# Optimization experiments

Measured on AMD Instinct MI355X. Metric: run time of the kernel, lower is better.

Reference implementation:

```python
import jax, jax.numpy as jnp
import numpy as np

B, N, D = 32, 4096, 256
K, Dc = 128, 64  # Dc = D_sq // K (per-cluster residual dim)
NEG_SLOPE = 0.01  # LeakyReLU default
EPS = 1e-12       # F.normalize default eps


def setup_inputs() -> dict:
    key = jax.random.key(0)
    ks = jax.random.split(key, 7)
    s = 0.05
    return {
        "descriptors": jax.random.normal(ks[0], (B, N, D), dtype=jnp.float32),
        # squeeze: Linear(D, Dc) -> LeakyReLU -> Linear(Dc, Dc)
        "W1": jax.random.normal(ks[1], (Dc, D), dtype=jnp.float32) * s,
        "b1": jnp.zeros((Dc,), dtype=jnp.float32),
        "W2": jax.random.normal(ks[2], (Dc, Dc), dtype=jnp.float32) * s,
        "b2": jnp.zeros((Dc,), dtype=jnp.float32),
        # assign: Linear(D, K) -> Softmax
        "Wa": jax.random.normal(ks[3], (K, D), dtype=jnp.float32) * s,
        "ba": jnp.zeros((K,), dtype=jnp.float32),
        # centroids (K, Dc)
        "centroid": jax.random.normal(ks[4], (K, Dc), dtype=jnp.float32),
    }


def reference(descriptors, W1, b1, W2, b2, Wa, ba, centroid):
    # squeeze MLP: (B,N,D) -> (B,N,Dc)
    h = jnp.einsum('bnd,ed->bne', descriptors, W1) + b1
    h = jnp.where(h >= 0, h, NEG_SLOPE * h)
    sq = jnp.einsum('bne,fe->bnf', h, W2) + b2
    # soft assignment: (B,N,K)
    assign = jax.nn.softmax(jnp.einsum('bnd,kd->bnk', descriptors, Wa) + ba, axis=-1)
    # VLAD: sum_n assign[b,n,k] * (sq[b,n,:] - centroid[k,:])
    # decomposed algebraically to avoid the (B,N,K,Dc) intermediate
    agg = jnp.einsum('bnd,bnk->bkd', sq, assign)          # (B,K,Dc)
    mass = assign.sum(axis=1)                              # (B,K)
    vlad = agg - mass[:, :, None] * centroid               # (B,K,Dc)
    out = vlad.reshape(B, K * Dc)
    norm = jnp.linalg.norm(out, axis=1, keepdims=True)
    return out / jnp.maximum(norm, EPS)
```

## Files before the change

kernel.cpp:

```cpp
#include <hip/hip_runtime.h>


#define B_   32
#define N_   4096
#define D_   256
#define K_   128
#define DC_  64
#define ITERS 16
#define NEG  0.01f

typedef __attribute__((ext_vector_type(8))) short bf16x8;
typedef __attribute__((ext_vector_type(4))) float f32x4;

#define XF_OFF   0
#define AT_OFF   16384
#define HB_OFF   24576
#define W2F_OFF  28672
#define MS_OFF   36864
#define LDS_BYTES 37888

__device__ __forceinline__ unsigned short f2bf(float x) {
  union { float f; unsigned u; } v; v.f = x;
  unsigned r = v.u + 0x7fffu + ((v.u >> 16) & 1u);
  return (unsigned short)(r >> 16);
}
__device__ __forceinline__ unsigned pack2(float a, float b) {
  return (unsigned)f2bf(a) | ((unsigned)f2bf(b) << 16);
}
__device__ __forceinline__ bf16x8 ldf(const char* s, int off) {
  return *reinterpret_cast<const bf16x8*>(s + off);
}

__global__ __launch_bounds__(512, 2)
void netvlad_phase1(const float* __restrict__ desc, const float* __restrict__ W1,
                    const float* __restrict__ b1, const float* __restrict__ W2,
                    const float* __restrict__ Wa, const float* __restrict__ ba,
                    float* __restrict__ agg, float* __restrict__ mass)
{
  extern __shared__ char smem[];
  const int t    = threadIdx.x;
  const int b    = blockIdx.x >> 3;
  const int blk  = blockIdx.x & 7;
  const int w    = t >> 6;
  const int lane = t & 63;
  const int li   = lane & 15;
  const int quad = lane >> 4;
  const int rt   = w >> 2;
  const int cg   = w & 3;
  const int nWa  = (cg < 2) ? 3 : (cg == 2 ? 2 : 0);

  {
    int L = t & 63;
    int row = ((t >> 7) << 4) + (L & 15);
    int col = (((t >> 6) & 1) << 5) + ((L >> 4) << 3);
    const float* src = W2 + row * DC_ + col;
    float4 a = *(const float4*)src, c = *(const float4*)(src + 4);
    uint4 o; o.x = pack2(a.x, a.y); o.y = pack2(a.z, a.w);
    o.z = pack2(c.x, c.y); o.w = pack2(c.z, c.w);
    *reinterpret_cast<uint4*>(smem + W2F_OFF + t * 16) = o;
  }

  bf16x8 wf[3][8];
  #pragma unroll
  for (int j = 0; j < 3; ++j) {
    const int g = cg * 3 + j;
    const float* wrow = (g < 8) ? (Wa + (size_t)(g * 16 + li) * D_)
                                : (W1 + (size_t)((g - 8) * 16 + li) * D_);
    #pragma unroll
    for (int ks = 0; ks < 8; ++ks) {
      const float* s = wrow + ks * 32 + quad * 8;
      float4 a = *(const float4*)s, c = *(const float4*)(s + 4);
      union { uint4 u; bf16x8 v; } cv;
      cv.u.x = pack2(a.x, a.y); cv.u.y = pack2(a.z, a.w);
      cv.u.z = pack2(c.x, c.y); cv.u.w = pack2(c.z, c.w);
      wf[j][ks] = cv.v;
    }
  }

  float biasr[3];
  #pragma unroll
  for (int j = 0; j < 3; ++j) {
    const int g = cg * 3 + j;
    biasr[j] = (g < 8) ? ba[g * 16 + li] : b1[(g - 8) * 16 + li];
  }

  float4 xp[4];
  auto issueX = [&](int itn) {
    const int n0 = blk * 512 + itn * 32;
    #pragma unroll
    for (int i = 0; i < 2; ++i) {
      int p = t + i * 512;
      int L = p & 63;
      const float* src = desc + ((size_t)b * N_ + n0 + ((p >> 9) << 4) + (L & 15)) * D_
                       + (((p >> 6) & 7) << 5) + ((L >> 4) << 3);
      xp[2 * i]     = *(const float4*)src;
      xp[2 * i + 1] = *(const float4*)(src + 4);
    }
  };
  auto writeX = [&]() {
    #pragma unroll
    for (int i = 0; i < 2; ++i) {
      uint4 o;
      o.x = pack2(xp[2 * i].x,     xp[2 * i].y);
      o.y = pack2(xp[2 * i].z,     xp[2 * i].w);
      o.z = pack2(xp[2 * i + 1].x, xp[2 * i + 1].y);
      o.w = pack2(xp[2 * i + 1].z, xp[2 * i + 1].w);
      *reinterpret_cast<uint4*>(smem + XF_OFF + (t + i * 512) * 16) = o;
    }
  };

  issueX(0); writeX(); issueX(1);

  f32x4 gacc[4];
  #pragma unroll
  for (int nt = 0; nt < 4; ++nt) gacc[nt] = (f32x4){0.f, 0.f, 0.f, 0.f};
  float massA[3] = {0.f, 0.f, 0.f};

  __syncthreads();

  for (int it = 0; it < ITERS; ++it) {
    f32x4 accT[3];
    #pragma unroll
    for (int j = 0; j < 3; ++j) accT[j] = (f32x4){0.f, 0.f, 0.f, 0.f};
    #pragma unroll
    for (int ks = 0; ks < 8; ++ks) {
      bf16x8 xa = ldf(smem, XF_OFF + ((rt * 8 + ks) * 64 + lane) * 16);
      #pragma unroll
      for (int j = 0; j < 3; ++j)
        accT[j] = __builtin_amdgcn_mfma_f32_16x16x32_bf16(xa, wf[j][ks], accT[j], 0, 0, 0);
    }
    #pragma unroll
    for (int j = 0; j < 3; ++j) {
      accT[j][0] += biasr[j]; accT[j][1] += biasr[j];
      accT[j][2] += biasr[j]; accT[j][3] += biasr[j];
    }

    float m4[4], s4[4];
    if (nWa) {
      #pragma unroll
      for (int r = 0; r < 4; ++r) {
        float m = -1e30f;
        #pragma unroll
        for (int j = 0; j < 3; ++j) if (j < nWa) m = fmaxf(m, accT[j][r]);
        #pragma unroll
        for (int off = 1; off < 16; off <<= 1) m = fmaxf(m, __shfl_xor(m, off, 64));
        float s = 0.f;
        #pragma unroll
        for (int j = 0; j < 3; ++j) if (j < nWa) {
          float e = __expf(accT[j][r] - m); accT[j][r] = e; s += e;
        }
        #pragma unroll
        for (int off = 1; off < 16; off <<= 1) s += __shfl_xor(s, off, 64);
        m4[r] = m; s4[r] = s;
      }
      if (li == 0) {
        #pragma unroll
        for (int r = 0; r < 4; ++r) {
          float2 v; v.x = m4[r]; v.y = s4[r];
          *reinterpret_cast<float2*>(smem + MS_OFF + ((rt * 4 + cg) * 16 + quad * 4 + r) * 8) = v;
        }
      }
    }
    __syncthreads();

    if (it + 1 < ITERS) { writeX(); if (it + 2 < ITERS) issueX(it + 2); }

    const int Lt  = li + 16 * (rt * 2 + (quad >> 1));
    const int sub = quad & 1;

    if (nWa) {
      const int g1 = (cg + 1) % 3, g2 = (cg + 2) % 3;
      float sc[4];
      #pragma unroll
      for (int r = 0; r < 4; ++r) {
        const int row = quad * 4 + r;
        float2 o1 = *reinterpret_cast<const float2*>(smem + MS_OFF + ((rt * 4 + g1) * 16 + row) * 8);
        float2 o2 = *reinterpret_cast<const float2*>(smem + MS_OFF + ((rt * 4 + g2) * 16 + row) * 8);
        float M  = fmaxf(m4[r], fmaxf(o1.x, o2.x));
        float e0 = __expf(m4[r] - M);
        float S  = s4[r] * e0 + o1.y * __expf(o1.x - M) + o2.y * __expf(o2.x - M);
        sc[r] = e0 / S;
      }
      #pragma unroll
      for (int j = 0; j < 3; ++j) if (j < nWa) {
        const int g = cg * 3 + j;
        float a0 = accT[j][0] * sc[0], a1 = accT[j][1] * sc[1];
        float a2 = accT[j][2] * sc[2], a3 = accT[j][3] * sc[3];
        massA[j] += a0 + a1 + a2 + a3;
        uint2 pk; pk.x = pack2(a0, a1); pk.y = pack2(a2, a3);
        *reinterpret_cast<uint2*>(smem + AT_OFF + g * 1024 + Lt * 16 + sub * 8) = pk;
      }
    }
    if (cg >= 2) {
      #pragma unroll
      for (int j = 0; j < 3; ++j) {
        const int g = cg * 3 + j;
        if (g >= 8) {
          const int ce = g - 8;
          float h0 = accT[j][0], h1 = accT[j][1], h2 = accT[j][2], h3 = accT[j][3];
          h0 = h0 >= 0.f ? h0 : NEG * h0;  h1 = h1 >= 0.f ? h1 : NEG * h1;
          h2 = h2 >= 0.f ? h2 : NEG * h2;  h3 = h3 >= 0.f ? h3 : NEG * h3;
          uint2 pk; pk.x = pack2(h0, h1); pk.y = pack2(h2, h3);
          *reinterpret_cast<uint2*>(smem + HB_OFF + ce * 1024 + Lt * 16 + sub * 8) = pk;
        }
      }
    }
    __syncthreads();

    bf16x8 af = ldf(smem, AT_OFF + w * 1024 + lane * 16);
    #pragma unroll
    for (int nt = 0; nt < 4; ++nt) {
      bf16x8 hb = ldf(smem, HB_OFF + nt * 1024 + lane * 16);
      gacc[nt] = __builtin_amdgcn_mfma_f32_16x16x32_bf16(af, hb, gacc[nt], 0, 0, 0);
    }
  }

  #pragma unroll
  for (int nt = 0; nt < 4; ++nt) {
    const int ke = nt >> 1;
    const int Lc = quad * 4 + 16 * (((nt & 1) << 1) + (li >> 3));
    const int jj = li & 7;
    #pragma unroll
    for (int r = 0; r < 4; ++r)
      *reinterpret_cast<unsigned short*>(
        smem + XF_OFF + (w * 2 + ke) * 1024 + (Lc + r) * 16 + jj * 2) = f2bf(gacc[nt][r]);
  }

  f32x4 wacc[4];
  #pragma unroll
  for (int nt = 0; nt < 4; ++nt) wacc[nt] = (f32x4){0.f, 0.f, 0.f, 0.f};
  #pragma unroll
  for (int ke = 0; ke < 2; ++ke) {
    bf16x8 uf = ldf(smem, XF_OFF + (w * 2 + ke) * 1024 + lane * 16);
    #pragma unroll
    for (int nt = 0; nt < 4; ++nt) {
      bf16x8 w2f = ldf(smem, W2F_OFF + ((nt * 2 + ke) * 64 + lane) * 16);
      wacc[nt] = __builtin_amdgcn_mfma_f32_16x16x32_bf16(uf, w2f, wacc[nt], 0, 0, 0);
    }
  }

  float* aggB = agg + (size_t)b * (K_ * DC_);
  #pragma unroll
  for (int nt = 0; nt < 4; ++nt)
    #pragma unroll
    for (int r = 0; r < 4; ++r)
      atomicAdd(&aggB[(w * 16 + quad * 4 + r) * DC_ + nt * 16 + li], wacc[nt][r]);

  #pragma unroll
  for (int j = 0; j < 3; ++j) if (j < nWa) {
    float v = massA[j];
    v += __shfl_xor(v, 16, 64);
    v += __shfl_xor(v, 32, 64);
    if (lane < 16) atomicAdd(&mass[b * K_ + (cg * 3 + j) * 16 + li], v);
  }
}

__global__ __launch_bounds__(1024)
void netvlad_phase2(const float* __restrict__ agg, const float* __restrict__ mass,
                    const float* __restrict__ b2, const float* __restrict__ centroid,
                    float* __restrict__ out)
{
  __shared__ float v[K_ * DC_];
  __shared__ float red[16];
  const int b = blockIdx.x, t = threadIdx.x;
  float ss = 0.f;
  for (int idx = t; idx < K_ * DC_; idx += 1024) {
    int k = idx >> 6, d = idx & 63;
    float val = agg[(size_t)b * K_ * DC_ + idx] + mass[b * K_ + k] * (b2[d] - centroid[idx]);
    v[idx] = val;
    ss += val * val;
  }
  #pragma unroll
  for (int off = 32; off > 0; off >>= 1) ss += __shfl_down(ss, off, 64);
  if ((t & 63) == 0) red[t >> 6] = ss;
  __syncthreads();
  if (t == 0) {
    float s = 0.f;
    #pragma unroll
    for (int i = 0; i < 16; ++i) s += red[i];
    red[0] = 1.0f / fmaxf(sqrtf(s), 1e-12f);
  }
  __syncthreads();
  float inv = red[0];
  for (int idx = t; idx < K_ * DC_; idx += 1024)
    out[(size_t)b * K_ * DC_ + idx] = v[idx] * inv;
}

extern "C" void kernel_launch(void* const* d_in, const int* in_sizes, int n_in,
                              void* d_out, int out_size, void* d_ws, size_t ws_size,
                              hipStream_t stream) {
  const float* desc     = (const float*)d_in[0];
  const float* W1       = (const float*)d_in[1];
  const float* b1       = (const float*)d_in[2];
  const float* W2       = (const float*)d_in[3];
  const float* b2       = (const float*)d_in[4];
  const float* Wa       = (const float*)d_in[5];
  const float* ba       = (const float*)d_in[6];
  const float* centroid = (const float*)d_in[7];
  float* out = (float*)d_out;

  float* agg  = (float*)d_ws;
  float* mass = agg + B_ * K_ * DC_;
  size_t zbytes = (size_t)(B_ * K_ * DC_ + B_ * K_) * sizeof(float);
  hipMemsetAsync(d_ws, 0, zbytes, stream);

  hipFuncSetAttribute(reinterpret_cast<const void*>(netvlad_phase1),
                      hipFuncAttributeMaxDynamicSharedMemorySize, LDS_BYTES);

  netvlad_phase1<<<dim3(B_ * 8), dim3(512), LDS_BYTES, stream>>>(
      desc, W1, b1, W2, Wa, ba, agg, mass);
  netvlad_phase2<<<dim3(B_), dim3(1024), 0, stream>>>(agg, mass, b2, centroid, out);
}
```

Before: 225.0 us.

## Restructure NetVLAD: per-wave row ownership, defer W2 to phase2, drop atomics

Each wave now owns 64 descriptor rows and computes the full softmax over all 128 clusters in registers. This removes the cross-wave max/sum exchange and the two block barriers per iteration. The W2 projection is moved after aggregation, using linearity (agg = (A^T h) W2^T + mass*b2), so phase1 accumulates an A^T h product of size Dc×K and phase2 applies W2 once per batch. Per-block partials are written to workspace and summed deterministically in phase2, replacing the atomics and the memset. Descriptors are loaded straight from global memory into MFMA fragments, with weights staged in a larger LDS. The costs are half-empty K=32 MFMAs for the outer product, much higher register pressure from 32 accumulators, and more LDS per block, which may lower occupancy.

```diff
diff --git a/kernel.cpp b/kernel.cpp
--- a/kernel.cpp
+++ b/kernel.cpp
@@ -6,18 +6,13 @@
 #define D_   256
 #define K_   128
 #define DC_  64
-#define ITERS 16
+#define ITERS 4
 #define NEG  0.01f
 
 typedef __attribute__((ext_vector_type(8))) short bf16x8;
 typedef __attribute__((ext_vector_type(4))) float f32x4;
 
-#define XF_OFF   0
-#define AT_OFF   16384
-#define HB_OFF   24576
-#define W2F_OFF  28672
-#define MS_OFF   36864
-#define LDS_BYTES 37888
+#define LDS_BYTES 98304
 
 __device__ __forceinline__ unsigned short f2bf(float x) {
   union { float f; unsigned u; } v; v.f = x;
@@ -30,12 +25,23 @@
 __device__ __forceinline__ bf16x8 ldf(const char* s, int off) {
   return *reinterpret_cast<const bf16x8*>(s + off);
 }
+__device__ __forceinline__ bf16x8 fragz(unsigned lo, unsigned hi) {
+  union { unsigned u[4]; bf16x8 v; } t;
+  t.u[0] = lo; t.u[1] = hi; t.u[2] = 0u; t.u[3] = 0u;
+  return t.v;
+}
+__device__ __forceinline__ bf16x8 pack8(float4 a, float4 c) {
+  union { unsigned u[4]; bf16x8 v; } t;
+  t.u[0] = pack2(a.x, a.y); t.u[1] = pack2(a.z, a.w);
+  t.u[2] = pack2(c.x, c.y); t.u[3] = pack2(c.z, c.w);
+  return t.v;
+}
 
 __global__ __launch_bounds__(512, 2)
 void netvlad_phase1(const float* __restrict__ desc, const float* __restrict__ W1,
-                    const float* __restrict__ b1, const float* __restrict__ W2,
-                    const float* __restrict__ Wa, const float* __restrict__ ba,
-                    float* __restrict__ agg, float* __restrict__ mass)
+                    const float* __restrict__ b1, const float* __restrict__ Wa,
+                    const float* __restrict__ ba,
+                    float* __restrict__ ws_u, float* __restrict__ ws_m)
 {
   extern __shared__ char smem[];
   const int t    = threadIdx.x;
@@ -44,232 +50,198 @@
   const int w    = t >> 6;
   const int lane = t & 63;
   const int li   = lane & 15;
-  const int quad = lane >> 4;
-  const int rt   = w >> 2;
-  const int cg   = w & 3;
-  const int nWa  = (cg < 2) ? 3 : (cg == 2 ? 2 : 0);
-
-  {
-    int L = t & 63;
-    int row = ((t >> 7) << 4) + (L & 15);
-    int col = (((t >> 6) & 1) << 5) + ((L >> 4) << 3);
-    const float* src = W2 + row * DC_ + col;
+  const int q    = lane >> 4;
+
+  for (int p = t; p < 6144; p += 512) {
+    int L = p & 63, ks = (p >> 6) & 7, g = p >> 9;
+    const float* src = (g < 8 ? Wa + (size_t)(g * 16 + (L & 15)) * D_
+                              : W1 + (size_t)((g - 8) * 16 + (L & 15)) * D_)
+                       + ks * 32 + ((L >> 4) << 3);
     float4 a = *(const float4*)src, c = *(const float4*)(src + 4);
-    uint4 o; o.x = pack2(a.x, a.y); o.y = pack2(a.z, a.w);
+    uint4 o;
+    o.x = pack2(a.x, a.y); o.y = pack2(a.z, a.w);
     o.z = pack2(c.x, c.y); o.w = pack2(c.z, c.w);
-    *reinterpret_cast<uint4*>(smem + W2F_OFF + t * 16) = o;
-  }
-
-  bf16x8 wf[3][8];
-  #pragma unroll
-  for (int j = 0; j < 3; ++j) {
-    const int g = cg * 3 + j;
-    const float* wrow = (g < 8) ? (Wa + (size_t)(g * 16 + li) * D_)
-                                : (W1 + (size_t)((g - 8) * 16 + li) * D_);
+    *reinterpret_cast<uint4*>(smem + ((g * 8 + ks) * 64 + L) * 16) = o;
+  }
+
+  float bar[8], b1r[4];
+  #pragma unroll
+  for (int kt = 0; kt < 8; ++kt) bar[kt] = ba[kt * 16 + li];
+  #pragma unroll
+  for (int et = 0; et < 4; ++et) b1r[et] = b1[et * 16 + li];
+
+  f32x4 uacc[4][8];
+  #pragma unroll
+  for (int et = 0; et < 4; ++et)
+    #pragma unroll
+    for (int kt = 0; kt < 8; ++kt) uacc[et][kt] = (f32x4){0.f, 0.f, 0.f, 0.f};
+  float mreg[8] = {0.f, 0.f, 0.f, 0.f, 0.f, 0.f, 0.f, 0.f};
+
+  __syncthreads();
+
+  const int rowb = blk * 512 + w * 64;
+  for (int it = 0; it < ITERS; ++it) {
+    const float* xb = desc + ((size_t)b * N_ + rowb + it * 16 + li) * D_ + q * 8;
+    bf16x8 xf[8];
     #pragma unroll
     for (int ks = 0; ks < 8; ++ks) {
-      const float* s = wrow + ks * 32 + quad * 8;
-      float4 a = *(const float4*)s, c = *(const float4*)(s + 4);
-      union { uint4 u; bf16x8 v; } cv;
-      cv.u.x = pack2(a.x, a.y); cv.u.y = pack2(a.z, a.w);
-      cv.u.z = pack2(c.x, c.y); cv.u.w = pack2(c.z, c.w);
-      wf[j][ks] = cv.v;
-    }
-  }
-
-  float biasr[3];
-  #pragma unroll
-  for (int j = 0; j < 3; ++j) {
-    const int g = cg * 3 + j;
-    biasr[j] = (g < 8) ? ba[g * 16 + li] : b1[(g - 8) * 16 + li];
-  }
-
-  float4 xp[4];
-  auto issueX = [&](int itn) {
-    const int n0 = blk * 512 + itn * 32;
-    #pragma unroll
-    for (int i = 0; i < 2; ++i) {
-      int p = t + i * 512;
-      int L = p & 63;
-      const float* src = desc + ((size_t)b * N_ + n0 + ((p >> 9) << 4) + (L & 15)) * D_
-                       + (((p >> 6) & 7) << 5) + ((L >> 4) << 3);
-      xp[2 * i]     = *(const float4*)src;
-      xp[2 * i + 1] = *(const float4*)(src + 4);
-    }
-  };
-  auto writeX = [&]() {
-    #pragma unroll
-    for (int i = 0; i < 2; ++i) {
-      uint4 o;
-      o.x = pack2(xp[2 * i].x,     xp[2 * i].y);
-      o.y = pack2(xp[2 * i].z,     xp[2 * i].w);
-      o.z = pack2(xp[2 * i + 1].x, xp[2 * i + 1].y);
-      o.w = pack2(xp[2 * i + 1].z, xp[2 * i + 1].w);
-      *reinterpret_cast<uint4*>(smem + XF_OFF + (t + i * 512) * 16) = o;
-    }
-  };
-
-  issueX(0); writeX(); issueX(1);
-
-  f32x4 gacc[4];
-  #pragma unroll
-  for (int nt = 0; nt < 4; ++nt) gacc[nt] = (f32x4){0.f, 0.f, 0.f, 0.f};
-  float massA[3] = {0.f, 0.f, 0.f};
-
-  __syncthreads();
-
-  for (int it = 0; it < ITERS; ++it) {
-    f32x4 accT[3];
-    #pragma unroll
-    for (int j = 0; j < 3; ++j) accT[j] = (f32x4){0.f, 0.f, 0.f, 0.f};
-    #pragma unroll
-    for (int ks = 0; ks < 8; ++ks) {
-      bf16x8 xa = ldf(smem, XF_OFF + ((rt * 8 + ks) * 64 + lane) * 16);
-      #pragma unroll
-      for (int j = 0; j < 3; ++j)
-        accT[j] = __builtin_amdgcn_mfma_f32_16x16x32_bf16(xa, wf[j][ks], accT[j], 0, 0, 0);
-    }
-    #pragma unroll
-    for (int j = 0; j < 3; ++j) {
-      accT[j][0] += biasr[j]; accT[j][1] += biasr[j];
-      accT[j][2] += biasr[j]; accT[j][3] += biasr[j];
-    }
-
-    float m4[4], s4[4];
-    if (nWa) {
-      #pragma unroll
-      for (int r = 0; r < 4; ++r) {
-        float m = -1e30f;
-        #pragma unroll
-        for (int j = 0; j < 3; ++j) if (j < nWa) m = fmaxf(m, accT[j][r]);
-        #pragma unroll
-        for (int off = 1; off < 16; off <<= 1) m = fmaxf(m, __shfl_xor(m, off, 64));
-        float s = 0.f;
-        #pragma unroll
-        for (int j = 0; j < 3; ++j) if (j < nWa) {
-          float e = __expf(accT[j][r] - m); accT[j][r] = e; s += e;
-        }
-        #pragma unroll
-        for (int off = 1; off < 16; off <<= 1) s += __shfl_xor(s, off, 64);
-        m4[r] = m; s4[r] = s;
+      float4 a = *(const float4*)(xb + ks * 32);
+      float4 c = *(const float4*)(xb + ks * 32 + 4);
+      xf[ks] = pack8(a, c);
+    }
+
+    f32x4 hh[4];
+    #pragma unroll
+    for (int et = 0; et < 4; ++et) hh[et] = (f32x4){0.f, 0.f, 0.f, 0.f};
+    #pragma unroll
+    for (int ks = 0; ks < 8; ++ks)
+      #pragma unroll
+      for (int et = 0; et < 4; ++et)
+        hh[et] = __builtin_amdgcn_mfma_f32_16x16x32_bf16(
+            xf[ks], ldf(smem, (((8 + et) * 8 + ks) * 64 + lane) * 16), hh[et], 0, 0, 0);
+    uint2 hpk[4];
+    #pragma unroll
+    for (int et = 0; et < 4; ++et) {
+      float v0 = hh[et][0] + b1r[et], v1 = hh[et][1] + b1r[et];
+      float v2 = hh[et][2] + b1r[et], v3 = hh[et][3] + b1r[et];
+      v0 = v0 >= 0.f ? v0 : NEG * v0;  v1 = v1 >= 0.f ? v1 : NEG * v1;
+      v2 = v2 >= 0.f ? v2 : NEG * v2;  v3 = v3 >= 0.f ? v3 : NEG * v3;
+      hpk[et].x = pack2(v0, v1); hpk[et].y = pack2(v2, v3);
+    }
+
+    f32x4 accL[8];
+    #pragma unroll
+    for (int kt = 0; kt < 8; ++kt) accL[kt] = (f32x4){0.f, 0.f, 0.f, 0.f};
+    #pragma unroll
+    for (int ks = 0; ks < 8; ++ks)
+      #pragma unroll
+      for (int kt = 0; kt < 8; ++kt)
+        accL[kt] = __builtin_amdgcn_mfma_f32_16x16x32_bf16(
+            xf[ks], ldf(smem, ((kt * 8 + ks) * 64 + lane) * 16), accL[kt], 0, 0, 0);
+    #pragma unroll
+    for (int kt = 0; kt < 8; ++kt) {
+      accL[kt][0] += bar[kt]; accL[kt][1] += bar[kt];
+      accL[kt][2] += bar[kt]; accL[kt][3] += bar[kt];
+    }
+
+    float inv4[4];
+    #pragma unroll
+    for (int r = 0; r < 4; ++r) {
+      float m = accL[0][r];
+      #pragma unroll
+      for (int kt = 1; kt < 8; ++kt) m = fmaxf(m, accL[kt][r]);
+      #pragma unroll
+      for (int off = 1; off < 16; off <<= 1) m = fmaxf(m, __shfl_xor(m, off, 64));
+      float s = 0.f;
+      #pragma unroll
+      for (int kt = 0; kt < 8; ++kt) {
+        float e = __expf(accL[kt][r] - m); accL[kt][r] = e; s += e;
       }
-      if (li == 0) {
-        #pragma unroll
-        for (int r = 0; r < 4; ++r) {
-          float2 v; v.x = m4[r]; v.y = s4[r];
-          *reinterpret_cast<float2*>(smem + MS_OFF + ((rt * 4 + cg) * 16 + quad * 4 + r) * 8) = v;
-        }
-      }
-    }
-    __syncthreads();
-
-    if (it + 1 < ITERS) { writeX(); if (it + 2 < ITERS) issueX(it + 2); }
-
-    const int Lt  = li + 16 * (rt * 2 + (quad >> 1));
-    const int sub = quad & 1;
-
-    if (nWa) {
-      const int g1 = (cg + 1) % 3, g2 = (cg + 2) % 3;
-      float sc[4];
-      #pragma unroll
-      for (int r = 0; r < 4; ++r) {
-        const int row = quad * 4 + r;
-        float2 o1 = *reinterpret_cast<const float2*>(smem + MS_OFF + ((rt * 4 + g1) * 16 + row) * 8);
-        float2 o2 = *reinterpret_cast<const float2*>(smem + MS_OFF + ((rt * 4 + g2) * 16 + row) * 8);
-        float M  = fmaxf(m4[r], fmaxf(o1.x, o2.x));
-        float e0 = __expf(m4[r] - M);
-        float S  = s4[r] * e0 + o1.y * __expf(o1.x - M) + o2.y * __expf(o2.x - M);
-        sc[r] = e0 / S;
-      }
-      #pragma unroll
-      for (int j = 0; j < 3; ++j) if (j < nWa) {
-        const int g = cg * 3 + j;
-        float a0 = accT[j][0] * sc[0], a1 = accT[j][1] * sc[1];
-        float a2 = accT[j][2] * sc[2], a3 = accT[j][3] * sc[3];
-        massA[j] += a0 + a1 + a2 + a3;
-        uint2 pk; pk.x = pack2(a0, a1); pk.y = pack2(a2, a3);
-        *reinterpret_cast<uint2*>(smem + AT_OFF + g * 1024 + Lt * 16 + sub * 8) = pk;
-      }
-    }
-    if (cg >= 2) {
-      #pragma unroll
-      for (int j = 0; j < 3; ++j) {
-        const int g = cg * 3 + j;
-        if (g >= 8) {
-          const int ce = g - 8;
-          float h0 = accT[j][0], h1 = accT[j][1], h2 = accT[j][2], h3 = accT[j][3];
-          h0 = h0 >= 0.f ? h0 : NEG * h0;  h1 = h1 >= 0.f ? h1 : NEG * h1;
-          h2 = h2 >= 0.f ? h2 : NEG * h2;  h3 = h3 >= 0.f ? h3 : NEG * h3;
-          uint2 pk; pk.x = pack2(h0, h1); pk.y = pack2(h2, h3);
-          *reinterpret_cast<uint2*>(smem + HB_OFF + ce * 1024 + Lt * 16 + sub * 8) = pk;
-        }
-      }
-    }
-    __syncthreads();
-
-    bf16x8 af = ldf(smem, AT_OFF + w * 1024 + lane * 16);
-    #pragma unroll
-    for (int nt = 0; nt < 4; ++nt) {
-      bf16x8 hb = ldf(smem, HB_OFF + nt * 1024 + lane * 16);
-      gacc[nt] = __builtin_amdgcn_mfma_f32_16x16x32_bf16(af, hb, gacc[nt], 0, 0, 0);
-    }
-  }
-
-  #pragma unroll
-  for (int nt = 0; nt < 4; ++nt) {
-    const int ke = nt >> 1;
-    const int Lc = quad * 4 + 16 * (((nt & 1) << 1) + (li >> 3));
-    const int jj = li & 7;
-    #pragma unroll
-    for (int r = 0; r < 4; ++r)
-      *reinterpret_cast<unsigned short*>(
-        smem + XF_OFF + (w * 2 + ke) * 1024 + (Lc + r) * 16 + jj * 2) = f2bf(gacc[nt][r]);
-  }
-
-  f32x4 wacc[4];
-  #pragma unroll
-  for (int nt = 0; nt < 4; ++nt) wacc[nt] = (f32x4){0.f, 0.f, 0.f, 0.f};
-  #pragma unroll
-  for (int ke = 0; ke < 2; ++ke) {
-    bf16x8 uf = ldf(smem, XF_OFF + (w * 2 + ke) * 1024 + lane * 16);
-    #pragma unroll
-    for (int nt = 0; nt < 4; ++nt) {
-      bf16x8 w2f = ldf(smem, W2F_OFF + ((nt * 2 + ke) * 64 + lane) * 16);
-      wacc[nt] = __builtin_amdgcn_mfma_f32_16x16x32_bf16(uf, w2f, wacc[nt], 0, 0, 0);
-    }
-  }
-
-  float* aggB = agg + (size_t)b * (K_ * DC_);
-  #pragma unroll
-  for (int nt = 0; nt < 4; ++nt)
-    #pragma unroll
-    for (int r = 0; r < 4; ++r)
-      atomicAdd(&aggB[(w * 16 + quad * 4 + r) * DC_ + nt * 16 + li], wacc[nt][r]);
-
-  #pragma unroll
-  for (int j = 0; j < 3; ++j) if (j < nWa) {
-    float v = massA[j];
+      #pragma unroll
+      for (int off = 1; off < 16; off <<= 1) s += __shfl_xor(s, off, 64);
+      inv4[r] = 1.0f / s;
+    }
+
+    #pragma unroll
+    for (int kt = 0; kt < 8; ++kt) {
+      float a0 = accL[kt][0] * inv4[0], a1 = accL[kt][1] * inv4[1];
+      float a2 = accL[kt][2] * inv4[2], a3 = accL[kt][3] * inv4[3];
+      mreg[kt] += a0 + a1 + a2 + a3;
+      bf16x8 af = fragz(pack2(a0, a1), pack2(a2, a3));
+      #pragma unroll
+      for (int et = 0; et < 4; ++et)
+        uacc[et][kt] = __builtin_amdgcn_mfma_f32_16x16x32_bf16(
+            fragz(hpk[et].x, hpk[et].y), af, uacc[et][kt], 0, 0, 0);
+    }
+  }
+
+  #pragma unroll
+  for (int kt = 0; kt < 8; ++kt) {
+    float v = mreg[kt];
     v += __shfl_xor(v, 16, 64);
     v += __shfl_xor(v, 32, 64);
-    if (lane < 16) atomicAdd(&mass[b * K_ + (cg * 3 + j) * 16 + li], v);
+    mreg[kt] = v;
+  }
+
+  const size_t obase = (size_t)(b * 8 + blk) * 4 * 2048;
+  for (int et = 0; et < 4; ++et) {
+    __syncthreads();
+    #pragma unroll
+    for (int kt = 0; kt < 8; ++kt)
+      *reinterpret_cast<f32x4*>(smem + ((w * 8 + kt) * 64 + lane) * 16) = uacc[et][kt];
+    if (et == 0 && lane < 16) {
+      #pragma unroll
+      for (int kt = 0; kt < 8; ++kt)
+        *reinterpret_cast<float*>(smem + 65536 + (w * 128 + kt * 16 + lane) * 4) = mreg[kt];
+    }
+    __syncthreads();
+    float4 s = {0.f, 0.f, 0.f, 0.f};
+    #pragma unroll
+    for (int p = 0; p < 8; ++p) {
+      float4 v = *reinterpret_cast<const float4*>(smem + p * 8192 + t * 16);
+      s.x += v.x; s.y += v.y; s.z += v.z; s.w += v.w;
+    }
+    *reinterpret_cast<float4*>(ws_u + obase + et * 2048 + t * 4) = s;
+    if (et == 0 && t < 128) {
+      float sm = 0.f;
+      #pragma unroll
+      for (int p = 0; p < 8; ++p)
+        sm += *reinterpret_cast<const float*>(smem + 65536 + (p * 128 + t) * 4);
+      ws_m[(b * 8 + blk) * 128 + t] = sm;
+    }
   }
 }
 
 __global__ __launch_bounds__(1024)
-void netvlad_phase2(const float* __restrict__ agg, const float* __restrict__ mass,
-                    const float* __restrict__ b2, const float* __restrict__ centroid,
-                    float* __restrict__ out)
+void netvlad_phase2(const float* __restrict__ ws_u, const float* __restrict__ ws_m,
+                    const float* __restrict__ W2, const float* __restrict__ b2,
+                    const float* __restrict__ centroid, float* __restrict__ out)
 {
-  __shared__ float v[K_ * DC_];
-  __shared__ float red[16];
+  __shared__ float u[DC_ * K_];
+  __shared__ float w2t[DC_ * DC_];
+  __shared__ float msh[K_];
+  __shared__ float red[17];
   const int b = blockIdx.x, t = threadIdx.x;
+
+  for (int idx = t; idx < 8192; idx += 1024) {
+    int et = idx >> 11, j = idx & 2047;
+    int kt = j >> 8, ln = (j >> 2) & 63, r = j & 3;
+    int e = et * 16 + (ln >> 4) * 4 + r, k = kt * 16 + (ln & 15);
+    float s = 0.f;
+    #pragma unroll
+    for (int p = 0; p < 8; ++p)
+      s += ws_u[((size_t)(b * 8 + p) * 4 + et) * 2048 + j];
+    u[e * K_ + k] = s;
+  }
+  for (int idx = t; idx < DC_ * DC_; idx += 1024)
+    w2t[(idx & 63) * 64 + (idx >> 6)] = W2[idx];
+  if (t < K_) {
+    float s = 0.f;
+    #pragma unroll
+    for (int p = 0; p < 8; ++p) s += ws_m[(b * 8 + p) * 128 + t];
+    msh[t] = s;
+  }
+  __syncthreads();
+
+  const int k = t >> 3, d0 = (t & 7) * 8;
+  float acc[8] = {0.f, 0.f, 0.f, 0.f, 0.f, 0.f, 0.f, 0.f};
+  #pragma unroll 8
+  for (int e = 0; e < DC_; ++e) {
+    float uk = u[e * K_ + k];
+    float4 wa = *(const float4*)&w2t[e * 64 + d0];
+    float4 wb = *(const float4*)&w2t[e * 64 + d0 + 4];
+    acc[0] += uk * wa.x; acc[1] += uk * wa.y; acc[2] += uk * wa.z; acc[3] += uk * wa.w;
+    acc[4] += uk * wb.x; acc[5] += uk * wb.y; acc[6] += uk * wb.z; acc[7] += uk * wb.w;
+  }
+  const float mk = msh[k];
+  const float* cb = centroid + k * 64 + d0;
+  const float* bb = b2 + d0;
+  #pragma unroll
+  for (int j = 0; j < 8; ++j) acc[j] += mk * (bb[j] - cb[j]);
+
   float ss = 0.f;
-  for (int idx = t; idx < K_ * DC_; idx += 1024) {
-    int k = idx >> 6, d = idx & 63;
-    float val = agg[(size_t)b * K_ * DC_ + idx] + mass[b * K_ + k] * (b2[d] - centroid[idx]);
-    v[idx] = val;
-    ss += val * val;
-  }
+  #pragma unroll
+  for (int j = 0; j < 8; ++j) ss += acc[j] * acc[j];
   #pragma unroll
   for (int off = 32; off > 0; off >>= 1) ss += __shfl_down(ss, off, 64);
   if ((t & 63) == 0) red[t >> 6] = ss;
@@ -278,12 +250,15 @@
     float s = 0.f;
     #pragma unroll
     for (int i = 0; i < 16; ++i) s += red[i];
-    red[0] = 1.0f / fmaxf(sqrtf(s), 1e-12f);
-  }
-  __syncthreads();
-  float inv = red[0];
-  for (int idx = t; idx < K_ * DC_; idx += 1024)
-    out[(size_t)b * K_ * DC_ + idx] = v[idx] * inv;
+    red[16] = 1.0f / fmaxf(sqrtf(s), 1e-12f);
+  }
+  __syncthreads();
+  const float inv = red[16];
+  float* op = out + (size_t)b * (K_ * DC_) + k * 64 + d0;
+  float4 o0 = {acc[0] * inv, acc[1] * inv, acc[2] * inv, acc[3] * inv};
+  float4 o1 = {acc[4] * inv, acc[5] * inv, acc[6] * inv, acc[7] * inv};
+  *reinterpret_cast<float4*>(op)     = o0;
+  *reinterpret_cast<float4*>(op + 4) = o1;
 }
 
 extern "C" void kernel_launch(void* const* d_in, const int* in_sizes, int n_in,
@@ -299,15 +274,14 @@
   const float* centroid = (const float*)d_in[7];
   float* out = (float*)d_out;
 
-  float* agg  = (float*)d_ws;
-  float* mass = agg + B_ * K_ * DC_;
-  size_t zbytes = (size_t)(B_ * K_ * DC_ + B_ * K_) * sizeof(float);
-  hipMemsetAsync(d_ws, 0, zbytes, stream);
+  float* ws_u = (float*)d_ws;
+  float* ws_m = ws_u + (size_t)B_ * 8 * 4 * 2048;
 
   hipFuncSetAttribute(reinterpret_cast<const void*>(netvlad_phase1),
                       hipFuncAttributeMaxDynamicSharedMemorySize, LDS_BYTES);
 
   netvlad_phase1<<<dim3(B_ * 8), dim3(512), LDS_BYTES, stream>>>(
-      desc, W1, b1, W2, Wa, ba, agg, mass);
-  netvlad_phase2<<<dim3(B_), dim3(1024), 0, stream>>>(agg, mass, b2, centroid, out);
-}
+      desc, W1, b1, Wa, ba, ws_u, ws_m);
+  netvlad_phase2<<<dim3(B_), dim3(1024), 0, stream>>>(
+      ws_u, ws_m, W2, b2, centroid, out);
+}
```

Measured after the change: 458.8 us. 104% more time.
